# Kernel optimization log

Measured on AMD Instinct MI355X. Metric: run time of the kernel, lower is better.

The kernel has to match this reference:

```python
import jax, jax.numpy as jnp
import numpy as np

ITERS_MAX = 10
MSE_THRESHOLD = 1e-05
CORR_THRESHOLD = 3.0
EPS = 1e-8


def setup_inputs() -> dict:
    key = jax.random.key(0)
    k1, k2 = jax.random.split(key)
    B, M = 16, 2048
    pc_src = jax.random.normal(k1, (B, 3, M), dtype=jnp.float32)
    pc_dest = jax.random.normal(k2, (B, 3, M), dtype=jnp.float32)
    mask = jnp.ones((B, M), dtype=bool)
    return {"pc_src": pc_src, "pc_dest": pc_dest, "pc_dest_is_valid_mask": mask}


def _icp(src, dest, valid):
    # src, dest: (B, 3, M); valid: (B, M) bool over dest points.
    B, _, M = src.shape
    dtype = src.dtype
    R0 = jnp.broadcast_to(jnp.eye(3, dtype=dtype), (B, 3, 3))
    t0 = jnp.zeros((B, 3), dtype=dtype)
    mse0 = jnp.zeros((B,), dtype=dtype)
    done0 = jnp.zeros((B,), dtype=bool)
    dest_sq = (dest * dest).sum(axis=1)  # (B, M)

    def body(i, carry):
        R, t, mse, done = carry
        # transform current source estimate
        p = jnp.einsum('bij,bjm->bim', R, src) + t[:, :, None]  # (B,3,M)
        # pairwise squared distances p (rows) vs dest (cols): (B, M, M)
        d2 = ((p * p).sum(axis=1)[:, :, None]
              + dest_sq[:, None, :]
              - 2.0 * jnp.einsum('bim,bin->bmn', p, dest))
        d2 = jnp.where(valid[:, None, :], d2, jnp.inf)
        nn_d2 = jnp.maximum(d2.min(axis=-1), 0.0)      # (B, M)
        nn_idx = d2.argmin(axis=-1)                    # (B, M)
        new_mse = nn_d2.mean(axis=-1)                  # (B,)
        # gather correspondences
        q = jnp.take_along_axis(dest, nn_idx[:, None, :], axis=2)  # (B,3,M)
        # reject far correspondences
        w = (jnp.sqrt(nn_d2) < CORR_THRESHOLD).astype(dtype)        # (B, M)
        wsum = w.sum(axis=-1, keepdims=True) + EPS                  # (B,1)
        mu_s = (src * w[:, None, :]).sum(axis=-1) / wsum            # (B,3)
        mu_q = (q * w[:, None, :]).sum(axis=-1) / wsum              # (B,3)
        sc = src - mu_s[:, :, None]
        qc = q - mu_q[:, :, None]
        # weighted cross-covariance, (B,3,3); Kabsch: H = sc W qc^T
        H = jnp.einsum('bim,bjm,bm->bij', sc, qc, w)
        U, S, Vt = jnp.linalg.svd(H)
        V = jnp.swapaxes(Vt, -1, -2)
        Ut = jnp.swapaxes(U, -1, -2)
        det = jnp.linalg.det(jnp.einsum('bij,bjk->bik', V, Ut))     # (B,)
        D = jnp.zeros((B, 3, 3), dtype=dtype)
        D = D.at[:, 0, 0].set(1.0).at[:, 1, 1].set(1.0).at[:, 2, 2].set(det)
        R_new = jnp.einsum('bij,bjk,bkl->bil', V, D, Ut)
        t_new = mu_q - jnp.einsum('bij,bj->bi', R_new, mu_s)
        # freeze batch items that already converged (early stopping)
        d3 = done[:, None, None]
        R_out = jnp.where(d3, R, R_new)
        t_out = jnp.where(done[:, None], t, t_new)
        mse_out = jnp.where(done, mse, new_mse)
        done_out = done | (new_mse < MSE_THRESHOLD)
        return (R_out, t_out, mse_out, done_out)

    R, t, mse, _ = jax.lax.fori_loop(0, ITERS_MAX, body, (R0, t0, mse0, done0))
    return R, t[:, :, None], mse[:, None]


def reference(pc_src, pc_dest, pc_dest_is_valid_mask):
    # R: (B,3,3), t: (B,3,1), mse: (B,1)
    return _icp(pc_src, pc_dest, pc_dest_is_valid_mask)
```

## Files before the change

### kernel.cpp

```cpp
#include <hip/hip_runtime.h>

#define B_ 16
#define M_ 2048
#define NBLK_PER_B 16
#define NW 16
#define THREADS 1024
#define ITERS 10
#define MSE_THR 1e-5f
#define EPS_ 1e-8f

#define CNT_STRIDE 32
#define PART_OFF 8192
#define PSTRIDE 20
#define ROWS_PER_B 32
#define PART_SZ (B_ * ROWS_PER_B * PSTRIDE)
#define ARRIVALS (2 * NBLK_PER_B)

typedef float f2 __attribute__((ext_vector_type(2)));

__device__ inline void kabsch_from_sums(const float* S, float Rn[3][3], float tn[3]) {
  float wsum = S[0] + EPS_;
  float inv = 1.f / wsum;
  float msv[3] = {S[1]*inv, S[2]*inv, S[3]*inv};
  float mqv[3] = {S[4]*inv, S[5]*inv, S[6]*inv};
  float h[3][3];
  for (int i = 0; i < 3; ++i)
    for (int j = 0; j < 3; ++j)
      h[i][j] = S[7+i*3+j] - msv[i]*S[4+j] - S[1+i]*mqv[j] + S[0]*msv[i]*mqv[j];

  float g[3][3], V[3][3];
  for (int i = 0; i < 3; ++i)
    for (int j = 0; j < 3; ++j) {
      g[i][j] = h[0][i]*h[0][j] + h[1][i]*h[1][j] + h[2][i]*h[2][j];
      V[i][j] = (i == j) ? 1.f : 0.f;
    }
  const int PP[3] = {0, 0, 1}, QQ[3] = {1, 2, 2};
  for (int sweep = 0; sweep < 6; ++sweep) {
    for (int r = 0; r < 3; ++r) {
      int p = PP[r], q = QQ[r];
      float apq = g[p][q];
      if (fabsf(apq) > 1e-30f) {
        float tau = (g[q][q] - g[p][p]) / (2.f * apq);
        float tt = (tau >= 0.f ? 1.f : -1.f) / (fabsf(tau) + sqrtf(1.f + tau*tau));
        float c = 1.f / sqrtf(1.f + tt*tt);
        float s = tt * c;
        for (int k = 0; k < 3; ++k) {
          float gkp = g[k][p], gkq = g[k][q];
          g[k][p] = c*gkp - s*gkq;
          g[k][q] = s*gkp + c*gkq;
        }
        for (int k = 0; k < 3; ++k) {
          float gpk = g[p][k], gqk = g[q][k];
          g[p][k] = c*gpk - s*gqk;
          g[q][k] = s*gpk + c*gqk;
        }
        for (int k = 0; k < 3; ++k) {
          float vkp = V[k][p], vkq = V[k][q];
          V[k][p] = c*vkp - s*vkq;
          V[k][q] = s*vkp + c*vkq;
        }
      }
    }
  }
  float lam[3] = {g[0][0], g[1][1], g[2][2]};
  for (int i = 0; i < 2; ++i)
    for (int j = i+1; j < 3; ++j)
      if (lam[i] < lam[j]) {
        float tl = lam[i]; lam[i] = lam[j]; lam[j] = tl;
        for (int k = 0; k < 3; ++k) { float tv = V[k][i]; V[k][i] = V[k][j]; V[k][j] = tv; }
      }
  float U[3][3];
  for (int k = 0; k < 3; ++k) {
    float ux = h[0][0]*V[0][k] + h[0][1]*V[1][k] + h[0][2]*V[2][k];
    float uy = h[1][0]*V[0][k] + h[1][1]*V[1][k] + h[1][2]*V[2][k];
    float uz = h[2][0]*V[0][k] + h[2][1]*V[1][k] + h[2][2]*V[2][k];
    float invs = 1.f / fmaxf(sqrtf(fmaxf(lam[k], 0.f)), 1e-20f);
    U[0][k] = ux*invs; U[1][k] = uy*invs; U[2][k] = uz*invs;
  }
  float detH = h[0][0]*(h[1][1]*h[2][2] - h[1][2]*h[2][1])
             - h[0][1]*(h[1][0]*h[2][2] - h[1][2]*h[2][0])
             + h[0][2]*(h[1][0]*h[2][1] - h[1][1]*h[2][0]);
  float d3 = (detH >= 0.f) ? 1.f : -1.f;
  for (int i = 0; i < 3; ++i)
    for (int j = 0; j < 3; ++j)
      Rn[i][j] = V[i][0]*U[j][0] + V[i][1]*U[j][1] + d3*V[i][2]*U[j][2];
  for (int i = 0; i < 3; ++i)
    tn[i] = mqv[i] - (Rn[i][0]*msv[0] + Rn[i][1]*msv[1] + Rn[i][2]*msv[2]);
}

__global__ void icp_init(unsigned* __restrict__ cnt) {
  int i = blockIdx.x * blockDim.x + threadIdx.x;
  if (i < B_ * ITERS * CNT_STRIDE) cnt[i] = 0u;
}

__global__ __launch_bounds__(THREADS, 2) void icp_fused(const float* __restrict__ src,
                                                        const float* __restrict__ dest,
                                                        float* __restrict__ ws,
                                                        float* __restrict__ out) {
  unsigned* cnt = (unsigned*)ws;
  float* partial = ws + PART_OFF;

  int blk = blockIdx.x;
  int b = blk >> 4, sub = blk & 15;
  int tid = threadIdx.x;
  int lane = tid & 63, w = tid >> 6;

  __shared__ float4 dt[M_];
  __shared__ float mval[NW][2][64];
  __shared__ int   midx[NW][2][64];
  __shared__ float Rsh[13];

#pragma unroll
  for (int k = 0; k < 2; ++k) {
    int n = tid + THREADS*k;
    float dx = dest[(b*3+0)*M_ + n];
    float dy = dest[(b*3+1)*M_ + n];
    float dz = dest[(b*3+2)*M_ + n];
    dt[n] = make_float4(dx, dy, dz, 0.5f*(dx*dx + dy*dy + dz*dz));
  }
  float sxr[2], syr[2], szr[2];
#pragma unroll
  for (int g = 0; g < 2; ++g) {
    int m = sub*128 + g*64 + lane;
    sxr[g] = src[(b*3+0)*M_ + m];
    syr[g] = src[(b*3+1)*M_ + m];
    szr[g] = src[(b*3+2)*M_ + m];
  }
  __syncthreads();

  float Rc[3][3] = {{1.f,0.f,0.f},{0.f,1.f,0.f},{0.f,0.f,1.f}};
  float tc[3] = {0.f, 0.f, 0.f};
  float mse = 0.f;
  bool done = false;

  const int sj0 = __builtin_amdgcn_readfirstlane(w) * 128;

  for (int it = 0; it < ITERS; ++it) {
    if (!done) {
      float npx[2], npy[2], npz[2];
      float psq0, psq1;
#pragma unroll
      for (int g = 0; g < 2; ++g) {
        float sx = sxr[g], sy = syr[g], sz = szr[g];
        float px = fmaf(Rc[0][0], sx, fmaf(Rc[0][1], sy, fmaf(Rc[0][2], sz, tc[0])));
        float py = fmaf(Rc[1][0], sx, fmaf(Rc[1][1], sy, fmaf(Rc[1][2], sz, tc[1])));
        float pz = fmaf(Rc[2][0], sx, fmaf(Rc[2][1], sy, fmaf(Rc[2][2], sz, tc[2])));
        npx[g] = -px; npy[g] = -py; npz[g] = -pz;
        float pq = px*px + py*py + pz*pz;
        if (g == 0) psq0 = pq; else psq1 = pq;
      }
      f2 npx2 = {npx[0], npx[1]};
      f2 npy2 = {npy[0], npy[1]};
      f2 npz2 = {npz[0], npz[1]};

      float bv0[4], bv1[4]; int bix0[4], bix1[4];
#pragma unroll
      for (int u = 0; u < 4; ++u) {
        bv0[u] = 3.0e38f; bv1[u] = 3.0e38f; bix0[u] = 0; bix1[u] = 0;
      }

#define NNS(D, IDX, U) do {                                                      \
        f2 vx = {(D).x, (D).x}, vy = {(D).y, (D).y};                             \
        f2 vz = {(D).z, (D).z}, vw = {(D).w, (D).w};                             \
        f2 aa = __builtin_elementwise_fma(npz2, vz,                              \
                 __builtin_elementwise_fma(npy2, vy,                             \
                  __builtin_elementwise_fma(npx2, vx, vw)));                     \
        bool l0 = aa.x < bv0[U];                                                 \
        bv0[U] = l0 ? aa.x : bv0[U]; bix0[U] = l0 ? (IDX) : bix0[U];             \
        bool l1 = aa.y < bv1[U];                                                 \
        bv1[U] = l1 ? aa.y : bv1[U]; bix1[U] = l1 ? (IDX) : bix1[U];             \
      } while (0)

      float4 A0=dt[sj0+0],  A1=dt[sj0+1],  A2=dt[sj0+2],  A3=dt[sj0+3];
      float4 A4=dt[sj0+4],  A5=dt[sj0+5],  A6=dt[sj0+6],  A7=dt[sj0+7];
      float4 B0=dt[sj0+8],  B1=dt[sj0+9],  B2=dt[sj0+10], B3=dt[sj0+11];
      float4 B4=dt[sj0+12], B5=dt[sj0+13], B6=dt[sj0+14], B7=dt[sj0+15];

      for (int j = 0; j < 128; j += 16) {
        const int jp = (j + 16) & 127;
        NNS(A0, sj0+j+0, 0);  NNS(A1, sj0+j+1, 1);
        NNS(A2, sj0+j+2, 2);  NNS(A3, sj0+j+3, 3);
        NNS(A4, sj0+j+4, 0);  NNS(A5, sj0+j+5, 1);
        NNS(A6, sj0+j+6, 2);  NNS(A7, sj0+j+7, 3);
        A0=dt[sj0+jp+0]; A1=dt[sj0+jp+1]; A2=dt[sj0+jp+2]; A3=dt[sj0+jp+3];
        A4=dt[sj0+jp+4]; A5=dt[sj0+jp+5]; A6=dt[sj0+jp+6]; A7=dt[sj0+jp+7];
        NNS(B0, sj0+j+8,  0); NNS(B1, sj0+j+9,  1);
        NNS(B2, sj0+j+10, 2); NNS(B3, sj0+j+11, 3);
        NNS(B4, sj0+j+12, 0); NNS(B5, sj0+j+13, 1);
        NNS(B6, sj0+j+14, 2); NNS(B7, sj0+j+15, 3);
        B0=dt[sj0+jp+8];  B1=dt[sj0+jp+9];  B2=dt[sj0+jp+10]; B3=dt[sj0+jp+11];
        B4=dt[sj0+jp+12]; B5=dt[sj0+jp+13]; B6=dt[sj0+jp+14]; B7=dt[sj0+jp+15];
      }
#undef NNS

      {
        float v = bv0[0]; int ix = bix0[0];
#pragma unroll
        for (int u = 1; u < 4; ++u) {
          bool better = (bv0[u] < v) || (bv0[u] == v && bix0[u] < ix);
          v = better ? bv0[u] : v;
          ix = better ? bix0[u] : ix;
        }
        mval[w][0][lane] = v; midx[w][0][lane] = ix;
      }
      {
        float v = bv1[0]; int ix = bix1[0];
#pragma unroll
        for (int u = 1; u < 4; ++u) {
          bool better = (bv1[u] < v) || (bv1[u] == v && bix1[u] < ix);
          v = better ? bv1[u] : v;
          ix = better ? bix1[u] : ix;
        }
        mval[w][1][lane] = v; midx[w][1][lane] = ix;
      }
      __syncthreads();

      unsigned* cptr = cnt + (b * ITERS + it) * CNT_STRIDE;

      if (w < 2) {
        float v = mval[0][w][lane]; int ix = midx[0][w][lane];
#pragma unroll
        for (int c = 1; c < NW; ++c) {
          float v2 = mval[c][w][lane]; int i2 = midx[c][w][lane];
          bool lt = v2 < v;
          v = lt ? v2 : v;
          ix = lt ? i2 : ix;
        }
        float psqg = (w == 0) ? psq0 : psq1;
        float sxg = (w == 0) ? sxr[0] : sxr[1];
        float syg = (w == 0) ? syr[0] : syr[1];
        float szg = (w == 0) ? szr[0] : szr[1];
        float nn = fmaxf(fmaf(2.f, v, psqg), 0.f);
        float a[17];
#pragma unroll
        for (int i = 0; i < 16; ++i) a[i] = 0.f;
        a[16] = nn;
        if (nn < 9.f) {
          float4 qd = dt[ix];
          a[0] = 1.f;
          a[1] = sxg; a[2] = syg; a[3] = szg;
          a[4] = qd.x; a[5] = qd.y; a[6] = qd.z;
          a[7]  = sxg*qd.x; a[8]  = sxg*qd.y; a[9]  = sxg*qd.z;
          a[10] = syg*qd.x; a[11] = syg*qd.y; a[12] = syg*qd.z;
          a[13] = szg*qd.x; a[14] = szg*qd.y; a[15] = szg*qd.z;
        }
#pragma unroll
        for (int i = 0; i < 17; ++i) {
          float vv = a[i];
          for (int off = 32; off > 0; off >>= 1) vv += __shfl_down(vv, off);
          a[i] = vv;
        }
        if (lane == 0) {
          float* pp = partial + (it & 1) * PART_SZ
                    + (b*ROWS_PER_B + sub*2 + w) * PSTRIDE;
#pragma unroll
          for (int i = 0; i < 17; ++i)
            __hip_atomic_store(pp + i, a[i], __ATOMIC_RELAXED, __HIP_MEMORY_SCOPE_AGENT);
        }
        asm volatile("s_waitcnt vmcnt(0)" ::: "memory");
        if (lane == 0)
          __hip_atomic_fetch_add(cptr, 1u, __ATOMIC_RELAXED, __HIP_MEMORY_SCOPE_AGENT);
      }

      if (w == 0) {
        if (lane == 0) {
          while (__hip_atomic_load(cptr, __ATOMIC_RELAXED, __HIP_MEMORY_SCOPE_AGENT)
                 < (unsigned)ARRIVALS)
            __builtin_amdgcn_s_sleep(1);
        }
        float vbuf[ROWS_PER_B];
        if (lane < 17) {
          const float* pp = partial + (it & 1) * PART_SZ;
#pragma unroll
          for (int c = 0; c < ROWS_PER_B; ++c)
            vbuf[c] = __hip_atomic_load(pp + (b*ROWS_PER_B + c)*PSTRIDE + lane,
                                        __ATOMIC_RELAXED, __HIP_MEMORY_SCOPE_AGENT);
        } else {
#pragma unroll
          for (int c = 0; c < ROWS_PER_B; ++c) vbuf[c] = 0.f;
        }
        float s = 0.f;
#pragma unroll
        for (int c = 0; c < ROWS_PER_B; ++c) s += vbuf[c];
        float S[17];
#pragma unroll
        for (int i = 0; i < 17; ++i) S[i] = __shfl(s, i);
        float Rn[3][3], tn[3];
        kabsch_from_sums(S, Rn, tn);
        if (lane == 0) {
          for (int i = 0; i < 3; ++i)
            for (int j = 0; j < 3; ++j) Rsh[i*3+j] = Rn[i][j];
          for (int i = 0; i < 3; ++i) Rsh[9+i] = tn[i];
          Rsh[12] = S[16] * (1.f / (float)M_);
        }
      }
      __syncthreads();
#pragma unroll
      for (int i = 0; i < 3; ++i) {
#pragma unroll
        for (int j = 0; j < 3; ++j) Rc[i][j] = Rsh[i*3+j];
        tc[i] = Rsh[9+i];
      }
      mse = Rsh[12];
      if (mse < MSE_THR) done = true;
    }
  }

  if (sub == 0 && tid == 0) {
#pragma unroll
    for (int i = 0; i < 3; ++i)
#pragma unroll
      for (int j = 0; j < 3; ++j) out[b*9 + i*3 + j] = Rc[i][j];
#pragma unroll
    for (int i = 0; i < 3; ++i) out[144 + b*3 + i] = tc[i];
    out[192 + b] = mse;
  }
}

extern "C" void kernel_launch(void* const* d_in, const int* in_sizes, int n_in,
                              void* d_out, int out_size, void* d_ws, size_t ws_size,
                              hipStream_t stream) {
  const float* src  = (const float*)d_in[0];
  const float* dest = (const float*)d_in[1];
  float* out = (float*)d_out;
  float* ws = (float*)d_ws;

  hipLaunchKernelGGL(icp_init, dim3((B_*ITERS*CNT_STRIDE + 255)/256), dim3(256), 0,
                     stream, (unsigned*)ws);

  void* args[] = { (void*)&src, (void*)&dest, (void*)&ws, (void*)&out };
  hipLaunchCooperativeKernel((void*)icp_fused, dim3(256), dim3(THREADS), args, 0, stream);
}
```

Measured before the change: 292.5 us.

## Split NN search so half the waves read dest from global memory instead of LDS

Waves 8-15 now stream destination coordinates straight from global memory (wave-uniform addresses, SoA float4 loads) and recompute the half squared norm on the fly. Waves 0-7 keep reading the packed float4 entries from shared memory. The aim is to split load traffic between the LDS and the scalar/vector memory path so the LDS bandwidth bottleneck shrinks. In exchange, those waves do extra ALU work per candidate and depend on cache hit rates. The half-norm is also computed in a different order, which can change nearest-neighbor tie behavior slightly.

```diff
diff --git a/kernel.cpp b/kernel.cpp
--- a/kernel.cpp
+++ b/kernel.cpp
@@ -133,7 +133,11 @@
   float mse = 0.f;
   bool done = false;
 
-  const int sj0 = __builtin_amdgcn_readfirstlane(w) * 128;
+  const int wu = __builtin_amdgcn_readfirstlane(w);
+  const int sj0 = wu * 128;
+  const float* bx = dest + (b*3+0)*M_ + sj0;
+  const float* by = bx + M_;
+  const float* bz = by + M_;
 
   for (int it = 0; it < ITERS; ++it) {
     if (!done) {
@@ -171,26 +175,68 @@
         bv1[U] = l1 ? aa.y : bv1[U]; bix1[U] = l1 ? (IDX) : bix1[U];             \
       } while (0)
 
-      float4 A0=dt[sj0+0],  A1=dt[sj0+1],  A2=dt[sj0+2],  A3=dt[sj0+3];
-      float4 A4=dt[sj0+4],  A5=dt[sj0+5],  A6=dt[sj0+6],  A7=dt[sj0+7];
-      float4 B0=dt[sj0+8],  B1=dt[sj0+9],  B2=dt[sj0+10], B3=dt[sj0+11];
-      float4 B4=dt[sj0+12], B5=dt[sj0+13], B6=dt[sj0+14], B7=dt[sj0+15];
-
-      for (int j = 0; j < 128; j += 16) {
-        const int jp = (j + 16) & 127;
-        NNS(A0, sj0+j+0, 0);  NNS(A1, sj0+j+1, 1);
-        NNS(A2, sj0+j+2, 2);  NNS(A3, sj0+j+3, 3);
-        NNS(A4, sj0+j+4, 0);  NNS(A5, sj0+j+5, 1);
-        NNS(A6, sj0+j+6, 2);  NNS(A7, sj0+j+7, 3);
-        A0=dt[sj0+jp+0]; A1=dt[sj0+jp+1]; A2=dt[sj0+jp+2]; A3=dt[sj0+jp+3];
-        A4=dt[sj0+jp+4]; A5=dt[sj0+jp+5]; A6=dt[sj0+jp+6]; A7=dt[sj0+jp+7];
-        NNS(B0, sj0+j+8,  0); NNS(B1, sj0+j+9,  1);
-        NNS(B2, sj0+j+10, 2); NNS(B3, sj0+j+11, 3);
-        NNS(B4, sj0+j+12, 0); NNS(B5, sj0+j+13, 1);
-        NNS(B6, sj0+j+14, 2); NNS(B7, sj0+j+15, 3);
-        B0=dt[sj0+jp+8];  B1=dt[sj0+jp+9];  B2=dt[sj0+jp+10]; B3=dt[sj0+jp+11];
-        B4=dt[sj0+jp+12]; B5=dt[sj0+jp+13]; B6=dt[sj0+jp+14]; B7=dt[sj0+jp+15];
-      }
+#define GNNS(X, Y, Z, JB) do {                                                   \
+        float w0 = 0.5f*((X).x*(X).x + (Y).x*(Y).x + (Z).x*(Z).x);               \
+        float w1 = 0.5f*((X).y*(X).y + (Y).y*(Y).y + (Z).y*(Z).y);               \
+        float w2 = 0.5f*((X).z*(X).z + (Y).z*(Y).z + (Z).z*(Z).z);               \
+        float w3 = 0.5f*((X).w*(X).w + (Y).w*(Y).w + (Z).w*(Z).w);               \
+        float4 d0 = make_float4((X).x, (Y).x, (Z).x, w0);                        \
+        float4 d1 = make_float4((X).y, (Y).y, (Z).y, w1);                        \
+        float4 d2 = make_float4((X).z, (Y).z, (Z).z, w2);                        \
+        float4 d3_ = make_float4((X).w, (Y).w, (Z).w, w3);                       \
+        NNS(d0, (JB)+0, 0); NNS(d1, (JB)+1, 1);                                  \
+        NNS(d2, (JB)+2, 2); NNS(d3_, (JB)+3, 3);                                 \
+      } while (0)
+
+      if (w < 8) {
+        float4 A0=dt[sj0+0],  A1=dt[sj0+1],  A2=dt[sj0+2],  A3=dt[sj0+3];
+        float4 A4=dt[sj0+4],  A5=dt[sj0+5],  A6=dt[sj0+6],  A7=dt[sj0+7];
+        float4 B0=dt[sj0+8],  B1=dt[sj0+9],  B2=dt[sj0+10], B3=dt[sj0+11];
+        float4 B4=dt[sj0+12], B5=dt[sj0+13], B6=dt[sj0+14], B7=dt[sj0+15];
+
+        for (int j = 0; j < 128; j += 16) {
+          const int jp = (j + 16) & 127;
+          NNS(A0, sj0+j+0, 0);  NNS(A1, sj0+j+1, 1);
+          NNS(A2, sj0+j+2, 2);  NNS(A3, sj0+j+3, 3);
+          NNS(A4, sj0+j+4, 0);  NNS(A5, sj0+j+5, 1);
+          NNS(A6, sj0+j+6, 2);  NNS(A7, sj0+j+7, 3);
+          A0=dt[sj0+jp+0]; A1=dt[sj0+jp+1]; A2=dt[sj0+jp+2]; A3=dt[sj0+jp+3];
+          A4=dt[sj0+jp+4]; A5=dt[sj0+jp+5]; A6=dt[sj0+jp+6]; A7=dt[sj0+jp+7];
+          NNS(B0, sj0+j+8,  0); NNS(B1, sj0+j+9,  1);
+          NNS(B2, sj0+j+10, 2); NNS(B3, sj0+j+11, 3);
+          NNS(B4, sj0+j+12, 0); NNS(B5, sj0+j+13, 1);
+          NNS(B6, sj0+j+14, 2); NNS(B7, sj0+j+15, 3);
+          B0=dt[sj0+jp+8];  B1=dt[sj0+jp+9];  B2=dt[sj0+jp+10]; B3=dt[sj0+jp+11];
+          B4=dt[sj0+jp+12]; B5=dt[sj0+jp+13]; B6=dt[sj0+jp+14]; B7=dt[sj0+jp+15];
+        }
+      } else {
+        float4 XA0 = *(const float4*)(bx + 0), YA0 = *(const float4*)(by + 0),
+               ZA0 = *(const float4*)(bz + 0);
+        float4 XA1 = *(const float4*)(bx + 4), YA1 = *(const float4*)(by + 4),
+               ZA1 = *(const float4*)(bz + 4);
+        float4 XB0 = *(const float4*)(bx + 8), YB0 = *(const float4*)(by + 8),
+               ZB0 = *(const float4*)(bz + 8);
+        float4 XB1 = *(const float4*)(bx + 12), YB1 = *(const float4*)(by + 12),
+               ZB1 = *(const float4*)(bz + 12);
+
+        for (int j = 0; j < 128; j += 16) {
+          const int ja = (j + 16) & 127;
+          const int jb = (j + 24) & 127;
+          GNNS(XA0, YA0, ZA0, sj0+j+0);
+          GNNS(XA1, YA1, ZA1, sj0+j+4);
+          XA0 = *(const float4*)(bx + ja);     YA0 = *(const float4*)(by + ja);
+          ZA0 = *(const float4*)(bz + ja);
+          XA1 = *(const float4*)(bx + ja + 4); YA1 = *(const float4*)(by + ja + 4);
+          ZA1 = *(const float4*)(bz + ja + 4);
+          GNNS(XB0, YB0, ZB0, sj0+j+8);
+          GNNS(XB1, YB1, ZB1, sj0+j+12);
+          XB0 = *(const float4*)(bx + jb);     YB0 = *(const float4*)(by + jb);
+          ZB0 = *(const float4*)(bz + jb);
+          XB1 = *(const float4*)(bx + jb + 4); YB1 = *(const float4*)(by + jb + 4);
+          ZB1 = *(const float4*)(bz + jb + 4);
+        }
+      }
+#undef GNNS
 #undef NNS
 
       {
```

Measured after the change: 329.8 us. 1.13x slower.
